# Optimization experiments

Hardware: AMD Instinct MI355X
Metric: run time of the kernel (lower is better)

Reference implementation:

```python
import jax, jax.numpy as jnp
import numpy as np

N = 50000

def gcn_conv(x, src, dst, W, b):
    # PyG GCNConv: h = x @ W; symmetric norm with self-loops; out = Ahat h + b
    h = x @ W  # [N, F]
    e = src.shape[0]
    deg = jax.ops.segment_sum(jnp.ones((e,), h.dtype), dst, num_segments=N) + 1.0  # +1 self-loop
    dinv = jax.lax.rsqrt(deg)  # deg >= 1 so finite
    norm = dinv[src] * dinv[dst]  # [E]
    agg = jax.ops.segment_sum(h[src] * norm[:, None], dst, num_segments=N)
    agg = agg + h * (dinv * dinv)[:, None]  # self-loop contribution
    return agg + b


def setup_inputs() -> dict:
    key = jax.random.key(0)
    ks = jax.random.split(key, 12)
    E = 400000
    x = jax.random.normal(ks[0], (N, 768), dtype=jnp.float32)
    edge_index = jax.random.randint(ks[1], (2, E), 0, N, dtype=jnp.int32)
    dims = [(768, 1536), (1536, 768), (768, 384), (384, 192), (192, 5)]
    inp = {"x": x, "edge_index": edge_index}
    for i, (fi, fo) in enumerate(dims):
        s = 1.0 / np.sqrt(fi)
        inp[f"W{i+1}"] = jax.random.uniform(ks[2 + 2 * i], (fi, fo), jnp.float32, -s, s)
        inp[f"b{i+1}"] = jnp.zeros((fo,), jnp.float32)
    return inp


def reference(x, edge_index, W1, b1, W2, b2, W3, b3, W4, b4, W5, b5):
    src, dst = edge_index[0], edge_index[1]
    h = x
    for W, b in [(W1, b1), (W2, b2), (W3, b3), (W4, b4)]:
        h = jax.nn.relu(gcn_conv(h, src, dst, W, b))
        # F.dropout with training=False is identity (eval mode)
    out = gcn_conv(h, src, dst, W5, b5)
    return (h, out)
```

## Files before the change

### kernel.cpp

```cpp
#include <hip/hip_runtime.h>
#include <stdint.h>

typedef unsigned short u16;
typedef unsigned int   u32;

#define NN 50000
#define NE 400000

typedef __bf16 bf16x8 __attribute__((ext_vector_type(8)));
typedef u16    u16x8  __attribute__((ext_vector_type(8)));
typedef float  f32x4  __attribute__((ext_vector_type(4)));

__device__ __forceinline__ float bf2f(u16 b) {
  union { u32 u; float f; } v; v.u = ((u32)b) << 16; return v.f;
}
__device__ __forceinline__ u16 f2bf(float f) {
  union { float f; u32 u; } v; v.f = f;
  u32 r = v.u + 0x7fffu + ((v.u >> 16) & 1u);
  return (u16)(r >> 16);
}


__global__ void zero_int_kernel(int* __restrict__ p, int n) {
  int i = blockIdx.x * blockDim.x + threadIdx.x;
  if (i < n) p[i] = 0;
}

__global__ void count_deg_kernel(const int* __restrict__ dst, int* __restrict__ deg, int e) {
  int i = blockIdx.x * blockDim.x + threadIdx.x;
  if (i < e) atomicAdd(&deg[dst[i]], 1);
}

__global__ void dinv_kernel(const int* __restrict__ deg, float* __restrict__ dinv, int n) {
  int i = blockIdx.x * blockDim.x + threadIdx.x;
  if (i < n) dinv[i] = rsqrtf((float)deg[i] + 1.0f);
}

__global__ __launch_bounds__(1024) void scan_kernel(const int* __restrict__ counts,
                                                    int* __restrict__ offsets, int n) {
  __shared__ int wsums[17];
  __shared__ int carry;
  int tid = threadIdx.x;
  int lane = tid & 63, wid = tid >> 6;
  if (tid == 0) carry = 0;
  __syncthreads();
  for (int base = 0; base < n; base += 1024) {
    int i = base + tid;
    int v = (i < n) ? counts[i] : 0;
    int s = v;
    #pragma unroll
    for (int off = 1; off < 64; off <<= 1) {
      int t = __shfl_up(s, off, 64);
      if (lane >= off) s += t;
    }
    if (lane == 63) wsums[wid] = s;
    __syncthreads();
    if (tid == 0) {
      int a = 0;
      #pragma unroll
      for (int w = 0; w < 16; ++w) { int t = wsums[w]; wsums[w] = a; a += t; }
      wsums[16] = a;
    }
    __syncthreads();
    if (i < n) offsets[i] = carry + wsums[wid] + s - v;
    __syncthreads();
    if (tid == 0) carry += wsums[16];
    __syncthreads();
  }
  if (tid == 0) offsets[n] = carry;
}

__global__ void csr_fill_kernel(const int* __restrict__ src, const int* __restrict__ dst,
                                const int* __restrict__ offsets, int* __restrict__ cursor,
                                const float* __restrict__ dinv,
                                int2* __restrict__ csr_pack, int e) {
  int i = blockIdx.x * blockDim.x + threadIdx.x;
  if (i < e) {
    int s = src[i], d = dst[i];
    int pos = offsets[d] + atomicAdd(&cursor[d], 1);
    float nr = dinv[s] * dinv[d];
    csr_pack[pos] = make_int2(s, __float_as_int(nr));
  }
}

__global__ void f2bf_kernel(const float* __restrict__ in, u16* __restrict__ out, int n) {
  int i = blockIdx.x * blockDim.x + threadIdx.x;
  if (i < n) out[i] = f2bf(in[i]);
}

__global__ void wt_kernel(const float* __restrict__ W, u16* __restrict__ Wt, int K, int N) {
  int i = blockIdx.x * blockDim.x + threadIdx.x;
  if (i < K * N) {
    int k = i / N;
    int n2 = i - k * N;
    Wt[n2 * K + k] = f2bf(W[i]);
  }
}


template<int G, bool HAS_BIAS, bool RELU, bool OUT_BF, bool OUT_F32>
__global__ __launch_bounds__(256) void agg8_kernel(
    const u16* __restrict__ g, const int* __restrict__ rowptr,
    const int2* __restrict__ csr_pack,
    const float* __restrict__ dinv, const float* __restrict__ bias,
    u16* __restrict__ outb, float* __restrict__ outf)
{
  constexpr int F = G * 8;
  int idx = blockIdx.x * blockDim.x + threadIdx.x;
  if (idx >= NN * G) return;
  int v = idx / G;
  int g8 = idx - v * G;
  const u16* base = g + g8 * 8;

  float acc[8];
  #pragma unroll
  for (int k = 0; k < 8; ++k) acc[k] = 0.f;

  int e0 = rowptr[v], e1 = rowptr[v + 1];
  int e = e0;
  for (; e + 1 < e1; e += 2) {
    int2 p0 = csr_pack[e];
    int2 p1 = csr_pack[e + 1];
    u16x8 r0 = *(const u16x8*)(base + (size_t)p0.x * F);
    u16x8 r1 = *(const u16x8*)(base + (size_t)p1.x * F);
    float n0 = __int_as_float(p0.y);
    float n1 = __int_as_float(p1.y);
    #pragma unroll
    for (int k = 0; k < 8; ++k) acc[k] += n0 * bf2f(r0[k]);
    #pragma unroll
    for (int k = 0; k < 8; ++k) acc[k] += n1 * bf2f(r1[k]);
  }
  if (e < e1) {
    int2 p0 = csr_pack[e];
    u16x8 r0 = *(const u16x8*)(base + (size_t)p0.x * F);
    float n0 = __int_as_float(p0.y);
    #pragma unroll
    for (int k = 0; k < 8; ++k) acc[k] += n0 * bf2f(r0[k]);
  }

  float sv = dinv[v]; sv *= sv;
  u16x8 sr = *(const u16x8*)(base + (size_t)v * F);
  float vals[8];
  #pragma unroll
  for (int k = 0; k < 8; ++k) {
    float val = acc[k] + sv * bf2f(sr[k]);
    if (HAS_BIAS) val += bias[g8 * 8 + k];
    if (RELU) val = fmaxf(val, 0.f);
    vals[k] = val;
  }
  if (OUT_BF) {
    u16x8 ob;
    #pragma unroll
    for (int k = 0; k < 8; ++k) ob[k] = f2bf(vals[k]);
    *(u16x8*)(outb + (size_t)v * F + g8 * 8) = ob;
  }
  if (OUT_F32) {
    f32x4 o0, o1;
    #pragma unroll
    for (int k = 0; k < 4; ++k) { o0[k] = vals[k]; o1[k] = vals[4 + k]; }
    float* op = outf + (size_t)v * F + g8 * 8;
    *(f32x4*)op = o0;
    *(f32x4*)(op + 4) = o1;
  }
}

__global__ void agg_small_kernel(const u16* __restrict__ g, const int* __restrict__ rowptr,
                                 const int2* __restrict__ csr_pack,
                                 const float* __restrict__ dinv, const float* __restrict__ bias,
                                 float* __restrict__ out, int n, int F) {
  int idx = blockIdx.x * blockDim.x + threadIdx.x;
  if (idx >= n * F) return;
  int v = idx / F;
  int f = idx - v * F;
  float acc = 0.f;
  int e1 = rowptr[v + 1];
  for (int e = rowptr[v]; e < e1; ++e) {
    int2 p = csr_pack[e];
    acc += __int_as_float(p.y) * bf2f(g[p.x * F + f]);
  }
  float dv = dinv[v];
  out[idx] = acc + dv * dv * bf2f(g[v * F + f]) + bias[f];
}


#define BM 128
#define BN 128
#define BK 32

__device__ __forceinline__ void gl_lds16(const void* g, void* l) {
  __builtin_amdgcn_global_load_lds((const __attribute__((address_space(1))) void*)g,
                                   (__attribute__((address_space(3))) void*)l, 16, 0, 0);
}

template<bool BIAS_RELU>
__global__ __launch_bounds__(256) void gemm_bt_kernel(
    const u16* __restrict__ A, const u16* __restrict__ Bt,
    u16* __restrict__ C, const float* __restrict__ bias,
    int M, int N, int K)
{
  __shared__ u16 As[BM * BK];
  __shared__ u16 Bs[BN * BK];
  int tid = threadIdx.x;
  int wave = tid >> 6, lane = tid & 63;
  int wm = wave & 1, wn = wave >> 1;
  int bm = blockIdx.x * BM, bn = blockIdx.y * BN;

  int srow = tid >> 2;
  int squad = tid & 3;
  int ar0 = min(bm + srow, M - 1);
  int ar1 = min(bm + 64 + srow, M - 1);
  int br0 = min(bn + srow, N - 1);
  int br1 = min(bn + 64 + srow, N - 1);
  const u16* ag0 = A + (size_t)ar0 * K + squad * 8;
  const u16* ag1 = A + (size_t)ar1 * K + squad * 8;
  const u16* bg0 = Bt + (size_t)br0 * K + squad * 8;
  const u16* bg1 = Bt + (size_t)br1 * K + squad * 8;
  u16* la0 = As + (wave * 16) * BK;
  u16* la1 = As + (64 + wave * 16) * BK;
  u16* lb0 = Bs + (wave * 16) * BK;
  u16* lb1 = Bs + (64 + wave * 16) * BK;

  f32x4 acc[4][4];
  #pragma unroll
  for (int i = 0; i < 4; ++i)
    #pragma unroll
    for (int j = 0; j < 4; ++j)
      acc[i][j] = (f32x4){0.f, 0.f, 0.f, 0.f};

  int row16 = lane & 15, q = lane >> 4;
  const u16* ard = As + (wm * 64 + row16) * BK + q * 8;
  const u16* brd = Bs + (wn * 64 + row16) * BK + q * 8;

  for (int k0 = 0; k0 < K; k0 += BK) {
    gl_lds16(ag0 + k0, la0);
    gl_lds16(ag1 + k0, la1);
    gl_lds16(bg0 + k0, lb0);
    gl_lds16(bg1 + k0, lb1);
    __syncthreads();
    bf16x8 af[4], bf[4];
    #pragma unroll
    for (int i = 0; i < 4; ++i) af[i] = *(const bf16x8*)(ard + i * 16 * BK);
    #pragma unroll
    for (int j = 0; j < 4; ++j) bf[j] = *(const bf16x8*)(brd + j * 16 * BK);
    #pragma unroll
    for (int i = 0; i < 4; ++i)
      #pragma unroll
      for (int j = 0; j < 4; ++j)
        acc[i][j] = __builtin_amdgcn_mfma_f32_16x16x32_bf16(af[i], bf[j], acc[i][j], 0, 0, 0);
    __syncthreads();
  }

  #pragma unroll
  for (int i = 0; i < 4; ++i) {
    int rbase = bm + wm * 64 + i * 16 + q * 4;
    #pragma unroll
    for (int j = 0; j < 4; ++j) {
      int col = bn + wn * 64 + j * 16 + row16;
      if (col < N) {
        float bv = BIAS_RELU ? bias[col] : 0.f;
        #pragma unroll
        for (int r = 0; r < 4; ++r) {
          int gr = rbase + r;
          if (gr < M) {
            float val = acc[i][j][r];
            if (BIAS_RELU) { val += bv; val = fmaxf(val, 0.f); }
            C[(size_t)gr * N + col] = f2bf(val);
          }
        }
      }
    }
  }
}


extern "C" void kernel_launch(void* const* d_in, const int* in_sizes, int n_in,
                              void* d_out, int out_size, void* d_ws, size_t ws_size,
                              hipStream_t stream) {
  const float* x   = (const float*)d_in[0];
  const int* ei    = (const int*)d_in[1];
  const int* src   = ei;
  const int* dst   = ei + NE;
  const float* W1  = (const float*)d_in[2];
  const float* b1  = (const float*)d_in[3];
  const float* W2  = (const float*)d_in[4];
  const float* b2  = (const float*)d_in[5];
  const float* W3  = (const float*)d_in[6];
  const float* b3  = (const float*)d_in[7];
  const float* W4  = (const float*)d_in[8];
  const float* b4  = (const float*)d_in[9];
  const float* W5  = (const float*)d_in[10];
  const float* b5  = (const float*)d_in[11];
  float* out_h = (float*)d_out;
  float* out_o = (float*)d_out + (size_t)NN * 192;

  char* p = (char*)d_ws;
  auto alloc = [&](size_t bytes) { char* r = p; p += (bytes + 255) & ~(size_t)255; return r; };
  int*   deg      = (int*)alloc((size_t)NN * 4);
  int*   cursor   = (int*)alloc((size_t)NN * 4);
  float* dinv     = (float*)alloc((size_t)NN * 4);
  int*   offs     = (int*)alloc((size_t)(NN + 1) * 4);
  int2*  csr_pack = (int2*)alloc((size_t)NE * 8);
  u16* W1t = (u16*)alloc((size_t)768 * 1536 * 2);
  u16* W2t = (u16*)alloc((size_t)1536 * 768 * 2);
  u16* W3t = (u16*)alloc((size_t)768 * 384 * 2);
  u16* W4t = (u16*)alloc((size_t)384 * 192 * 2);
  u16* W5t = (u16*)alloc((size_t)192 * 5 * 2);
  u16* B0 = (u16*)alloc((size_t)NN * 768 * 2);
  u16* B1 = (u16*)alloc((size_t)NN * 768 * 2);
  u16* B2 = (u16*)alloc((size_t)NN * 1536 * 2);

  u16* xb  = B0;
  u16* a0  = B1;
  u16* h1  = B2;
  u16* g2  = B0;
  u16* h2  = B1;
  u16* g3  = B0;
  u16* h3  = B2;
  u16* g4  = B0;
  u16* h4b = B1;
  u16* g5  = B0;

  const int M = NN;

  zero_int_kernel<<<(NN + 255) / 256, 256, 0, stream>>>(deg, NN);
  zero_int_kernel<<<(NN + 255) / 256, 256, 0, stream>>>(cursor, NN);
  count_deg_kernel<<<(NE + 255) / 256, 256, 0, stream>>>(dst, deg, NE);
  dinv_kernel<<<(NN + 255) / 256, 256, 0, stream>>>(deg, dinv, NN);
  scan_kernel<<<1, 1024, 0, stream>>>(deg, offs, NN);
  csr_fill_kernel<<<(NE + 255) / 256, 256, 0, stream>>>(src, dst, offs, cursor, dinv,
                                                        csr_pack, NE);
  f2bf_kernel<<<((NN * 768) + 255) / 256, 256, 0, stream>>>(x, xb, NN * 768);
  wt_kernel<<<((768 * 1536) + 255) / 256, 256, 0, stream>>>(W1, W1t, 768, 1536);
  wt_kernel<<<((1536 * 768) + 255) / 256, 256, 0, stream>>>(W2, W2t, 1536, 768);
  wt_kernel<<<((768 * 384) + 255) / 256, 256, 0, stream>>>(W3, W3t, 768, 384);
  wt_kernel<<<((384 * 192) + 255) / 256, 256, 0, stream>>>(W4, W4t, 384, 192);
  wt_kernel<<<((192 * 5) + 255) / 256, 256, 0, stream>>>(W5, W5t, 192, 5);

  dim3 blk(256);

  agg8_kernel<96, false, false, true, false><<<(NN * 96 + 255) / 256, blk, 0, stream>>>(
      xb, offs, csr_pack, dinv, nullptr, a0, nullptr);
  gemm_bt_kernel<true><<<dim3((M + BM - 1) / BM, 1536 / BN), blk, 0, stream>>>(
      a0, W1t, h1, b1, M, 1536, 768);

  gemm_bt_kernel<false><<<dim3((M + BM - 1) / BM, 768 / BN), blk, 0, stream>>>(
      h1, W2t, g2, nullptr, M, 768, 1536);
  agg8_kernel<96, true, true, true, false><<<(NN * 96 + 255) / 256, blk, 0, stream>>>(
      g2, offs, csr_pack, dinv, b2, h2, nullptr);

  gemm_bt_kernel<false><<<dim3((M + BM - 1) / BM, 384 / BN), blk, 0, stream>>>(
      h2, W3t, g3, nullptr, M, 384, 768);
  agg8_kernel<48, true, true, true, false><<<(NN * 48 + 255) / 256, blk, 0, stream>>>(
      g3, offs, csr_pack, dinv, b3, h3, nullptr);

  gemm_bt_kernel<false><<<dim3((M + BM - 1) / BM, (192 + BN - 1) / BN), blk, 0, stream>>>(
      h3, W4t, g4, nullptr, M, 192, 384);
  agg8_kernel<24, true, true, true, true><<<(NN * 24 + 255) / 256, blk, 0, stream>>>(
      g4, offs, csr_pack, dinv, b4, h4b, out_h);

  gemm_bt_kernel<false><<<dim3((M + BM - 1) / BM, 1), blk, 0, stream>>>(
      h4b, W5t, g5, nullptr, M, 5, 192);
  agg_small_kernel<<<((NN * 5) + 255) / 256, 256, 0, stream>>>(
      g5, offs, csr_pack, dinv, b5, out_o, NN, 5);
}
```

Before: 1.211 ms.

## Swizzle GEMM LDS layout, remap blocks per XCD, unroll gather by four

The GEMM moves to a 1D grid whose block index is remapped so each XCD handles a contiguous set of M-row tiles, which should improve L2 locality of the shared weight tiles. LDS k-chunks are rotated per row pair, matching the global-load source chunk to the read permutation, to reduce bank conflicts on fragment loads. The aggregation gather loop is unrolled to four edges to keep more memory loads in flight. In exchange, the padded grid launches some blocks that exit immediately, and the wider unroll adds register pressure.

```diff
diff --git a/kernel.cpp b/kernel.cpp
--- a/kernel.cpp
+++ b/kernel.cpp
@@ -118,19 +118,27 @@
 
   int e0 = rowptr[v], e1 = rowptr[v + 1];
   int e = e0;
-  for (; e + 1 < e1; e += 2) {
+  for (; e + 3 < e1; e += 4) {
     int2 p0 = csr_pack[e];
     int2 p1 = csr_pack[e + 1];
+    int2 p2 = csr_pack[e + 2];
+    int2 p3 = csr_pack[e + 3];
     u16x8 r0 = *(const u16x8*)(base + (size_t)p0.x * F);
     u16x8 r1 = *(const u16x8*)(base + (size_t)p1.x * F);
-    float n0 = __int_as_float(p0.y);
-    float n1 = __int_as_float(p1.y);
+    u16x8 r2 = *(const u16x8*)(base + (size_t)p2.x * F);
+    u16x8 r3 = *(const u16x8*)(base + (size_t)p3.x * F);
+    float n0 = __int_as_float(p0.y), n1 = __int_as_float(p1.y);
+    float n2 = __int_as_float(p2.y), n3 = __int_as_float(p3.y);
     #pragma unroll
     for (int k = 0; k < 8; ++k) acc[k] += n0 * bf2f(r0[k]);
     #pragma unroll
     for (int k = 0; k < 8; ++k) acc[k] += n1 * bf2f(r1[k]);
-  }
-  if (e < e1) {
+    #pragma unroll
+    for (int k = 0; k < 8; ++k) acc[k] += n2 * bf2f(r2[k]);
+    #pragma unroll
+    for (int k = 0; k < 8; ++k) acc[k] += n3 * bf2f(r3[k]);
+  }
+  for (; e < e1; ++e) {
     int2 p0 = csr_pack[e];
     u16x8 r0 = *(const u16x8*)(base + (size_t)p0.x * F);
     float n0 = __int_as_float(p0.y);
@@ -200,21 +208,31 @@
 {
   __shared__ u16 As[BM * BK];
   __shared__ u16 Bs[BN * BK];
+  int gm = (M + BM - 1) / BM;
+  int gn = (N + BN - 1) / BN;
+  int bid = blockIdx.x;
+  int xcd = bid & 7;
+  int t = bid >> 3;
+  int trow = t / gn;
+  int bn_i = t - trow * gn;
+  int row = trow * 8 + xcd;
+  if (row >= gm) return;
+  int bm = row * BM, bn = bn_i * BN;
+
   int tid = threadIdx.x;
   int wave = tid >> 6, lane = tid & 63;
   int wm = wave & 1, wn = wave >> 1;
-  int bm = blockIdx.x * BM, bn = blockIdx.y * BN;
 
   int srow = tid >> 2;
-  int squad = tid & 3;
+  int sq_log = ((tid & 3) - ((tid >> 3) & 3)) & 3;
   int ar0 = min(bm + srow, M - 1);
   int ar1 = min(bm + 64 + srow, M - 1);
   int br0 = min(bn + srow, N - 1);
   int br1 = min(bn + 64 + srow, N - 1);
-  const u16* ag0 = A + (size_t)ar0 * K + squad * 8;
-  const u16* ag1 = A + (size_t)ar1 * K + squad * 8;
-  const u16* bg0 = Bt + (size_t)br0 * K + squad * 8;
-  const u16* bg1 = Bt + (size_t)br1 * K + squad * 8;
+  const u16* ag0 = A + (size_t)ar0 * K + sq_log * 8;
+  const u16* ag1 = A + (size_t)ar1 * K + sq_log * 8;
+  const u16* bg0 = Bt + (size_t)br0 * K + sq_log * 8;
+  const u16* bg1 = Bt + (size_t)br1 * K + sq_log * 8;
   u16* la0 = As + (wave * 16) * BK;
   u16* la1 = As + (64 + wave * 16) * BK;
   u16* lb0 = Bs + (wave * 16) * BK;
@@ -228,8 +246,9 @@
       acc[i][j] = (f32x4){0.f, 0.f, 0.f, 0.f};
 
   int row16 = lane & 15, q = lane >> 4;
-  const u16* ard = As + (wm * 64 + row16) * BK + q * 8;
-  const u16* brd = Bs + (wn * 64 + row16) * BK + q * 8;
+  int perm = (q + (row16 >> 1)) & 3;
+  const u16* ard = As + (wm * 64 + row16) * BK + perm * 8;
+  const u16* brd = Bs + (wn * 64 + row16) * BK + perm * 8;
 
   for (int k0 = 0; k0 < K; k0 += BK) {
     gl_lds16(ag0 + k0, la0);
@@ -270,6 +289,13 @@
       }
     }
   }
+}
+
+static inline int gemm_grid(int M, int N) {
+  int gm = (M + BM - 1) / BM;
+  int gn = (N + BN - 1) / BN;
+  int rows_per_xcd = (gm + 7) / 8;
+  return rows_per_xcd * gn * 8;
 }
 
 
@@ -340,25 +366,25 @@
 
   agg8_kernel<96, false, false, true, false><<<(NN * 96 + 255) / 256, blk, 0, stream>>>(
       xb, offs, csr_pack, dinv, nullptr, a0, nullptr);
-  gemm_bt_kernel<true><<<dim3((M + BM - 1) / BM, 1536 / BN), blk, 0, stream>>>(
+  gemm_bt_kernel<true><<<gemm_grid(M, 1536), blk, 0, stream>>>(
       a0, W1t, h1, b1, M, 1536, 768);
 
-  gemm_bt_kernel<false><<<dim3((M + BM - 1) / BM, 768 / BN), blk, 0, stream>>>(
+  gemm_bt_kernel<false><<<gemm_grid(M, 768), blk, 0, stream>>>(
       h1, W2t, g2, nullptr, M, 768, 1536);
   agg8_kernel<96, true, true, true, false><<<(NN * 96 + 255) / 256, blk, 0, stream>>>(
       g2, offs, csr_pack, dinv, b2, h2, nullptr);
 
-  gemm_bt_kernel<false><<<dim3((M + BM - 1) / BM, 384 / BN), blk, 0, stream>>>(
+  gemm_bt_kernel<false><<<gemm_grid(M, 384), blk, 0, stream>>>(
       h2, W3t, g3, nullptr, M, 384, 768);
   agg8_kernel<48, true, true, true, false><<<(NN * 48 + 255) / 256, blk, 0, stream>>>(
       g3, offs, csr_pack, dinv, b3, h3, nullptr);
 
-  gemm_bt_kernel<false><<<dim3((M + BM - 1) / BM, (192 + BN - 1) / BN), blk, 0, stream>>>(
+  gemm_bt_kernel<false><<<gemm_grid(M, 192), blk, 0, stream>>>(
       h3, W4t, g4, nullptr, M, 192, 384);
   agg8_kernel<24, true, true, true, true><<<(NN * 24 + 255) / 256, blk, 0, stream>>>(
       g4, offs, csr_pack, dinv, b4, h4b, out_h);
 
-  gemm_bt_kernel<false><<<dim3((M + BM - 1) / BM, 1), blk, 0, stream>>>(
+  gemm_bt_kernel<false><<<gemm_grid(M, 5), blk, 0, stream>>>(
       h4b, W5t, g5, nullptr, M, 5, 192);
   agg_small_kernel<<<((NN * 5) + 255) / 256, 256, 0, stream>>>(
       g5, offs, csr_pack, dinv, b5, out_o, NN, 5);
```

After: 1.160 ms. 1.04x faster.
